# Kernel tuning notes

Measured on AMD Instinct MI355X. Metric: run time of the kernel, lower is better.

The kernel has to match this reference:

```python
import jax, jax.numpy as jnp
import numpy as np

B, T, VT, E, D = 128, 512, 2048, 1024, 1024  # batch, num_topics, topic_vocab, enc_hid, dec_hid


def setup_inputs() -> dict:
    key = jax.random.key(0)
    ks = jax.random.split(key, 8)
    # Split the Linear weight (in = dec_hid + topic_vocab + enc_hid, concat order: hidden, topic, enc)
    # into per-input blocks; math is identical to Linear(cat([h, t, e])).
    s = 1.0 / np.sqrt(D + VT + E)
    return {
        "hidden": jax.random.normal(ks[0], (B, D), jnp.float32),
        "topic_dict": jax.random.uniform(ks[1], (T, VT), jnp.float32),
        "enc_hidden": jax.random.normal(ks[2], (B, E), jnp.float32),
        "W_h": jax.random.uniform(ks[3], (D, D), jnp.float32, -s, s),
        "W_t": jax.random.uniform(ks[4], (VT, D), jnp.float32, -s, s),
        "W_e": jax.random.uniform(ks[5], (E, D), jnp.float32, -s, s),
        "b": jax.random.uniform(ks[6], (D,), jnp.float32, -s, s),
        "v": jax.random.uniform(ks[7], (D,), jnp.float32),
    }


def reference(hidden, topic_dict, enc_hidden, W_h, W_t, W_e, b, v):
    # Decompose Linear(cat(h, t, e)) = h@W_h + t@W_t + e@W_e + b; avoids the
    # repeated/concatenated [B, T, D+VT+E] buffer while computing the same math.
    h_proj = hidden @ W_h          # [B, D]
    t_proj = topic_dict @ W_t      # [T, D]
    e_proj = enc_hidden @ W_e      # [B, D]
    energy = jnp.tanh(h_proj[:, None, :] + e_proj[:, None, :] + t_proj[None, :, :] + b)  # [B, T, D]
    score = jnp.einsum("btd,d->bt", energy, v)  # [B, T]
    return jax.nn.softmax(score, axis=1)[:, None, :]  # [B, 1, T]
```

## Files before the change

### kernel.cpp

```cpp
#include <hip/hip_runtime.h>
#include <hip/hip_fp16.h>

#define B_ 128
#define T_ 512
#define VT_ 2048
#define E_ 1024
#define D_ 1024

typedef _Float16 h8 __attribute__((ext_vector_type(8)));
typedef float f4 __attribute__((ext_vector_type(4)));

#define C2LE 2.8853900817779268f
#define L2E  1.4426950408889634f

static __device__ __forceinline__ float rcpf(float x) { return __builtin_amdgcn_rcpf(x); }
static __device__ __forceinline__ float ex2(float x)  { return __builtin_amdgcn_exp2f(x); }

#define P_FLOATS   (8 * 640 * 1024)
#define R_FLOATS   (640 * 1024)
#define SP_FLOATS  (8 * 128 * 512)
#define PA_HALVES  (640 * 2048)
#define PB_WH      0
#define PB_WE      1048576
#define PB_WT      2097152

__device__ __forceinline__ void packA_do(const float* __restrict__ src, int ld, int KBs,
                                         _Float16* __restrict__ dst, int mb_off, int kb_off, int t)
{
    const int lane = t & 63;
    const int fb = t >> 6;
    const int kb = fb % KBs, mb = fb / KBs;
    const int r = lane & 15, g = lane >> 4;
    const float* s = src + (size_t)(mb * 16 + r) * ld + kb * 32 + g * 8;
    f4 v0 = *(const f4*)s, v1 = *(const f4*)(s + 4);
    h8 h;
    h[0] = (_Float16)v0[0]; h[1] = (_Float16)v0[1]; h[2] = (_Float16)v0[2]; h[3] = (_Float16)v0[3];
    h[4] = (_Float16)v1[0]; h[5] = (_Float16)v1[1]; h[6] = (_Float16)v1[2]; h[7] = (_Float16)v1[3];
    *(h8*)(dst + ((size_t)((mb_off + mb) * 64 + (kb_off + kb)) * 64 + lane) * 8) = h;
}

__device__ __forceinline__ void packB_do(const float* __restrict__ W, int KB,
                                         _Float16* __restrict__ dst, int t)
{
    const int lane = t & 63;
    const int fb = t >> 6;
    const int kb = fb % KB, nb = fb / KB;
    const int r = lane & 15, g = lane >> 4;
    const float* s = W + (size_t)(kb * 32 + g * 8) * 1024 + nb * 16 + r;
    h8 h;
    #pragma unroll
    for (int j = 0; j < 8; ++j) h[j] = (_Float16)s[(size_t)j * 1024];
    *(h8*)(dst + ((size_t)(nb * KB + kb) * 64 + lane) * 8) = h;
}

__global__ __launch_bounds__(256) void pack_kernel(
    const float* __restrict__ hidden, const float* __restrict__ topic,
    const float* __restrict__ enc,
    const float* __restrict__ W_h, const float* __restrict__ W_t, const float* __restrict__ W_e,
    _Float16* __restrict__ pA, _Float16* __restrict__ pB)
{
    const int bid = blockIdx.x, tid = threadIdx.x;
    if      (bid <   64) packA_do(hidden, 1024, 32, pA, 0,  0, bid * 256 + tid);
    else if (bid <  128) packA_do(enc,    1024, 32, pA, 0, 32, (bid -  64) * 256 + tid);
    else if (bid <  640) packA_do(topic,  2048, 64, pA, 8,  0, (bid - 128) * 256 + tid);
    else if (bid < 1152) packB_do(W_h, 32, pB + PB_WH, (bid -  640) * 256 + tid);
    else if (bid < 1664) packB_do(W_e, 32, pB + PB_WE, (bid - 1152) * 256 + tid);
    else                 packB_do(W_t, 64, pB + PB_WT, (bid - 1664) * 256 + tid);
}

__global__ __launch_bounds__(256, 3) void gemm_kernel(const _Float16* __restrict__ pA,
                                                      const _Float16* __restrict__ pB,
                                                      float* __restrict__ P)
{
    const int lin = blockIdx.x;
    const int sw  = (lin & 7) * 80 + (lin >> 3);
    const int s   = sw / 80;
    const int rem = sw % 80;
    const int mt  = rem % 10;
    const int nt  = rem / 10;

    const int tid = threadIdx.x, wave = tid >> 6, lane = tid & 63;
    const int wm = (wave >> 1) * 32;
    const int wn = (wave & 1) * 64;
    const int r = lane & 15, g = lane >> 4;

    const int mb0 = mt * 4 + (wm >> 4);
    const int nb0 = (nt * 128 + wn) >> 4;
    const int kb0 = s * 8;

    const _Float16* Bp; int KB_B, kbB0;
    if (mt < 2) {
        if (kb0 < 32) { Bp = pB + PB_WH; kbB0 = kb0; }
        else          { Bp = pB + PB_WE; kbB0 = kb0 - 32; }
        KB_B = 32;
    } else { Bp = pB + PB_WT; kbB0 = kb0; KB_B = 64; }

    const _Float16* Ap = pA + ((size_t)(mb0 * 64 + kb0) * 64 + lane) * 8;
    const _Float16* Bq = Bp + ((size_t)(nb0 * KB_B + kbB0) * 64 + lane) * 8;
    const size_t aStrM = (size_t)64 * 512;
    const size_t bStrN = (size_t)KB_B * 512;

    f4 acc[2][4] = {};
    #pragma unroll
    for (int ks = 0; ks < 8; ++ks) {
        h8 a0 = *(const h8*)(Ap + (size_t)ks * 512);
        h8 a1 = *(const h8*)(Ap + aStrM + (size_t)ks * 512);
        h8 b0 = *(const h8*)(Bq + (size_t)ks * 512);
        h8 b1 = *(const h8*)(Bq + bStrN + (size_t)ks * 512);
        h8 b2 = *(const h8*)(Bq + 2 * bStrN + (size_t)ks * 512);
        h8 b3 = *(const h8*)(Bq + 3 * bStrN + (size_t)ks * 512);
        acc[0][0] = __builtin_amdgcn_mfma_f32_16x16x32_f16(a0, b0, acc[0][0], 0, 0, 0);
        acc[0][1] = __builtin_amdgcn_mfma_f32_16x16x32_f16(a0, b1, acc[0][1], 0, 0, 0);
        acc[0][2] = __builtin_amdgcn_mfma_f32_16x16x32_f16(a0, b2, acc[0][2], 0, 0, 0);
        acc[0][3] = __builtin_amdgcn_mfma_f32_16x16x32_f16(a0, b3, acc[0][3], 0, 0, 0);
        acc[1][0] = __builtin_amdgcn_mfma_f32_16x16x32_f16(a1, b0, acc[1][0], 0, 0, 0);
        acc[1][1] = __builtin_amdgcn_mfma_f32_16x16x32_f16(a1, b1, acc[1][1], 0, 0, 0);
        acc[1][2] = __builtin_amdgcn_mfma_f32_16x16x32_f16(a1, b2, acc[1][2], 0, 0, 0);
        acc[1][3] = __builtin_amdgcn_mfma_f32_16x16x32_f16(a1, b3, acc[1][3], 0, 0, 0);
    }

    float* Pp = P + ((size_t)s * 640 + mt * 64 + wm + g * 4) * 1024 + nt * 128 + wn + r;
    #pragma unroll
    for (int i = 0; i < 2; ++i)
        #pragma unroll
        for (int j = 0; j < 4; ++j)
            #pragma unroll
            for (int q = 0; q < 4; ++q)
                Pp[(size_t)(i * 16 + q) * 1024 + j * 16] = C2LE * acc[i][j][q];
}

__global__ __launch_bounds__(256) void reduce_kernel(const float* __restrict__ P,
                                                     const float* __restrict__ bias,
                                                     float* __restrict__ R)
{
    const int row = blockIdx.x, tid = threadIdx.x;
    const size_t off = (size_t)row * 1024 + tid * 4;
    const size_t PS = (size_t)640 * 1024;
    f4 acc = *(const f4*)&P[off];
    #pragma unroll
    for (int z = 1; z < 8; ++z) acc += *(const f4*)&P[off + (size_t)z * PS];
    if (row < 128) {
        f4 bb = *(const f4*)&bias[tid * 4];
        acc += bb * C2LE;
    }
    *(f4*)&R[off] = acc;
}

__global__ __launch_bounds__(256) void score_kernel(const float* __restrict__ R,
                                                    const float* __restrict__ v,
                                                    float* __restrict__ SP)
{
    __shared__ float Xs[16][128];
    __shared__ float Ys[64][128];
    __shared__ float vs[128];

    const int tid = threadIdx.x;
    const int b0 = blockIdx.x * 16;
    const int t0 = blockIdx.y * 64;
    const int d0 = blockIdx.z * 128;

    #pragma unroll
    for (int i = 0; i < 8; ++i) {
        int idx = tid + i * 256;
        int row = idx >> 5, c4 = idx & 31;
        f4 vv = *(const f4*)&R[(size_t)(128 + t0 + row) * 1024 + d0 + c4 * 4];
        *(f4*)&Ys[row][(c4 ^ (row & 15)) * 4] = vv;
    }
    #pragma unroll
    for (int i = 0; i < 2; ++i) {
        int idx = tid + i * 256;
        int row = idx >> 5, c4 = idx & 31;
        f4 vv = *(const f4*)&R[(size_t)(b0 + row) * 1024 + d0 + c4 * 4];
        *(f4*)&Xs[row][(c4 ^ (row & 15)) * 4] = vv;
    }
    if (tid < 32) *(f4*)&vs[tid * 4] = *(const f4*)&v[d0 + tid * 4];
    __syncthreads();

    const int tq = tid & 31, bq = tid >> 5;
    const int sx0 = bq & 15, sx1 = (bq + 8) & 15, sy = tq & 15;
    float a00 = 0.f, a01 = 0.f, a10 = 0.f, a11 = 0.f;

    for (int dd = 0; dd < 32; ++dd) {
        f4 xa = *(const f4*)&Xs[bq]     [(dd ^ sx0) * 4];
        f4 xb = *(const f4*)&Xs[bq + 8] [(dd ^ sx1) * 4];
        f4 ya = *(const f4*)&Ys[tq]     [(dd ^ sy) * 4];
        f4 yb = *(const f4*)&Ys[tq + 32][(dd ^ sy) * 4];
        f4 vv = *(const f4*)&vs[dd * 4];
        #pragma unroll
        for (int j = 0; j < 4; ++j) {
            float e;
            e = ex2(xa[j] + ya[j]); a00 += vv[j] * rcpf(e + 1.0f);
            e = ex2(xa[j] + yb[j]); a01 += vv[j] * rcpf(e + 1.0f);
            e = ex2(xb[j] + ya[j]); a10 += vv[j] * rcpf(e + 1.0f);
            e = ex2(xb[j] + yb[j]); a11 += vv[j] * rcpf(e + 1.0f);
        }
    }

    float* sp = SP + (size_t)blockIdx.z * (B_ * T_);
    sp[(size_t)(b0 + bq)     * T_ + t0 + tq]      = a00;
    sp[(size_t)(b0 + bq)     * T_ + t0 + tq + 32] = a01;
    sp[(size_t)(b0 + bq + 8) * T_ + t0 + tq]      = a10;
    sp[(size_t)(b0 + bq + 8) * T_ + t0 + tq + 32] = a11;
}

__global__ __launch_bounds__(256) void softmax_kernel(
    const float* __restrict__ SP, float* __restrict__ out)
{
    const int b = blockIdx.x, tid = threadIdx.x;
    float s0 = 0.f, s1 = 0.f;
    #pragma unroll
    for (int z = 0; z < 8; ++z) {
        s0 += SP[(size_t)z * B_ * T_ + (size_t)b * T_ + tid];
        s1 += SP[(size_t)z * B_ * T_ + (size_t)b * T_ + tid + 256];
    }
    s0 *= -2.0f; s1 *= -2.0f;

    float m = fmaxf(s0, s1);
    #pragma unroll
    for (int off = 32; off >= 1; off >>= 1) m = fmaxf(m, __shfl_xor(m, off));
    __shared__ float red[4];
    __shared__ float red2[4];
    const int wv = tid >> 6;
    if ((tid & 63) == 0) red[wv] = m;
    __syncthreads();
    m = fmaxf(fmaxf(red[0], red[1]), fmaxf(red[2], red[3]));

    float e0 = ex2((s0 - m) * L2E);
    float e1 = ex2((s1 - m) * L2E);
    float sum = e0 + e1;
    #pragma unroll
    for (int off = 32; off >= 1; off >>= 1) sum += __shfl_xor(sum, off);
    if ((tid & 63) == 0) red2[wv] = sum;
    __syncthreads();
    sum = red2[0] + red2[1] + red2[2] + red2[3];

    const float rs = rcpf(sum);
    out[(size_t)b * T_ + tid]       = e0 * rs;
    out[(size_t)b * T_ + tid + 256] = e1 * rs;
}

extern "C" void kernel_launch(void* const* d_in, const int* in_sizes, int n_in,
                              void* d_out, int out_size, void* d_ws, size_t ws_size,
                              hipStream_t stream)
{
    const float* hidden = (const float*)d_in[0];
    const float* topic  = (const float*)d_in[1];
    const float* enc    = (const float*)d_in[2];
    const float* W_h    = (const float*)d_in[3];
    const float* W_t    = (const float*)d_in[4];
    const float* W_e    = (const float*)d_in[5];
    const float* bvec   = (const float*)d_in[6];
    const float* vvec   = (const float*)d_in[7];
    float* out = (float*)d_out;

    float* P      = (float*)d_ws;
    float* R      = P + P_FLOATS;
    float* SPb    = R + R_FLOATS;
    _Float16* pA  = (_Float16*)(SPb + SP_FLOATS);
    _Float16* pB  = pA + PA_HALVES;

    pack_kernel<<<2688, 256, 0, stream>>>(hidden, topic, enc, W_h, W_t, W_e, pA, pB);
    gemm_kernel<<<640, 256, 0, stream>>>(pA, pB, P);
    reduce_kernel<<<640, 256, 0, stream>>>(P, bvec, R);
    score_kernel<<<dim3(8, 8, 8), 256, 0, stream>>>(R, vvec, SPb);
    softmax_kernel<<<128, 256, 0, stream>>>(SPb, out);
}
```

Before: 115.0 us.

## Replace split-K partial buffer with atomic accumulation and LDS-staged packing

The GEMM's eight split-K slices now atomically add into a zeroed result buffer instead of writing separate partials, which removes the reduce kernel and its read of the partial buffer. The bias add moves into the score kernel. The pack kernel stages 64x64 panels through shared memory so both the A and weight conversions read global memory coalesced, rather than doing strided column reads for the weights. Costs are a memset launch, contention on the float atomics, and a summation order that is no longer deterministic.

After: 124.5 us. +8.3%, slower.

```diff
diff --git a/kernel.cpp b/kernel.cpp
--- a/kernel.cpp
+++ b/kernel.cpp
@@ -16,7 +16,6 @@
 static __device__ __forceinline__ float rcpf(float x) { return __builtin_amdgcn_rcpf(x); }
 static __device__ __forceinline__ float ex2(float x)  { return __builtin_amdgcn_exp2f(x); }
 
-#define P_FLOATS   (8 * 640 * 1024)
 #define R_FLOATS   (640 * 1024)
 #define SP_FLOATS  (8 * 128 * 512)
 #define PA_HALVES  (640 * 2048)
@@ -24,33 +23,55 @@
 #define PB_WE      1048576
 #define PB_WT      2097152
 
-__device__ __forceinline__ void packA_do(const float* __restrict__ src, int ld, int KBs,
-                                         _Float16* __restrict__ dst, int mb_off, int kb_off, int t)
-{
-    const int lane = t & 63;
-    const int fb = t >> 6;
-    const int kb = fb % KBs, mb = fb / KBs;
-    const int r = lane & 15, g = lane >> 4;
-    const float* s = src + (size_t)(mb * 16 + r) * ld + kb * 32 + g * 8;
-    f4 v0 = *(const f4*)s, v1 = *(const f4*)(s + 4);
-    h8 h;
-    h[0] = (_Float16)v0[0]; h[1] = (_Float16)v0[1]; h[2] = (_Float16)v0[2]; h[3] = (_Float16)v0[3];
-    h[4] = (_Float16)v1[0]; h[5] = (_Float16)v1[1]; h[6] = (_Float16)v1[2]; h[7] = (_Float16)v1[3];
-    *(h8*)(dst + ((size_t)((mb_off + mb) * 64 + (kb_off + kb)) * 64 + lane) * 8) = h;
-}
-
-__device__ __forceinline__ void packB_do(const float* __restrict__ W, int KB,
-                                         _Float16* __restrict__ dst, int t)
-{
-    const int lane = t & 63;
-    const int fb = t >> 6;
-    const int kb = fb % KB, nb = fb / KB;
-    const int r = lane & 15, g = lane >> 4;
-    const float* s = W + (size_t)(kb * 32 + g * 8) * 1024 + nb * 16 + r;
-    h8 h;
-    #pragma unroll
-    for (int j = 0; j < 8; ++j) h[j] = (_Float16)s[(size_t)j * 1024];
-    *(h8*)(dst + ((size_t)(nb * KB + kb) * 64 + lane) * 8) = h;
+__device__ __forceinline__ void pack_panelA(const float* __restrict__ src, int ld,
+                                            _Float16* __restrict__ dst, int mb_off, int kb_off,
+                                            int pm, int pk, int tid, float lds[64][72])
+{
+    #pragma unroll
+    for (int p = 0; p < 4; ++p) {
+        int row = (tid >> 4) + p * 16, col = (tid & 15) * 4;
+        *(f4*)&lds[row][col] = *(const f4*)&src[(size_t)(pm * 64 + row) * ld + pk * 64 + col];
+    }
+    __syncthreads();
+    #pragma unroll
+    for (int w = 0; w < 2; ++w) {
+        int fl = w * 256 + tid;
+        int f = fl >> 6, lane = fl & 63;
+        int i = f >> 1, k2 = f & 1;
+        int r = lane & 15, g = lane >> 4;
+        const float* p = &lds[i * 16 + r][k2 * 32 + g * 8];
+        h8 h;
+        #pragma unroll
+        for (int j = 0; j < 8; ++j) h[j] = (_Float16)p[j];
+        int MB = mb_off + pm * 4 + i;
+        int KB = kb_off + pk * 2 + k2;
+        *(h8*)(dst + ((size_t)(MB * 64 + KB) * 64 + lane) * 8) = h;
+    }
+}
+
+__device__ __forceinline__ void pack_panelB(const float* __restrict__ W,
+                                            _Float16* __restrict__ dst, int KBdim,
+                                            int pk, int pn, int tid, float lds[64][72])
+{
+    #pragma unroll
+    for (int p = 0; p < 4; ++p) {
+        int row = (tid >> 4) + p * 16, col = (tid & 15) * 4;
+        *(f4*)&lds[row][col] = *(const f4*)&W[(size_t)(pk * 64 + row) * 1024 + pn * 64 + col];
+    }
+    __syncthreads();
+    #pragma unroll
+    for (int w = 0; w < 2; ++w) {
+        int fl = w * 256 + tid;
+        int f = fl >> 6, lane = fl & 63;
+        int j = f >> 1, i2 = f & 1;
+        int r = lane & 15, g = lane >> 4;
+        h8 h;
+        #pragma unroll
+        for (int jj = 0; jj < 8; ++jj) h[jj] = (_Float16)lds[i2 * 32 + g * 8 + jj][j * 16 + r];
+        int NB = pn * 4 + j;
+        int KB = pk * 2 + i2;
+        *(h8*)(dst + ((size_t)(NB * KBdim + KB) * 64 + lane) * 8) = h;
+    }
 }
 
 __global__ __launch_bounds__(256) void pack_kernel(
@@ -59,18 +80,26 @@
     const float* __restrict__ W_h, const float* __restrict__ W_t, const float* __restrict__ W_e,
     _Float16* __restrict__ pA, _Float16* __restrict__ pB)
 {
+    __shared__ float lds[64][72];
     const int bid = blockIdx.x, tid = threadIdx.x;
-    if      (bid <   64) packA_do(hidden, 1024, 32, pA, 0,  0, bid * 256 + tid);
-    else if (bid <  128) packA_do(enc,    1024, 32, pA, 0, 32, (bid -  64) * 256 + tid);
-    else if (bid <  640) packA_do(topic,  2048, 64, pA, 8,  0, (bid - 128) * 256 + tid);
-    else if (bid < 1152) packB_do(W_h, 32, pB + PB_WH, (bid -  640) * 256 + tid);
-    else if (bid < 1664) packB_do(W_e, 32, pB + PB_WE, (bid - 1152) * 256 + tid);
-    else                 packB_do(W_t, 64, pB + PB_WT, (bid - 1664) * 256 + tid);
+    if (bid < 32) {
+        int b = bid;        pack_panelA(hidden, 1024, pA, 0,  0, b >> 4, b & 15, tid, lds);
+    } else if (bid < 64) {
+        int b = bid - 32;   pack_panelA(enc,    1024, pA, 0, 32, b >> 4, b & 15, tid, lds);
+    } else if (bid < 320) {
+        int b = bid - 64;   pack_panelA(topic,  2048, pA, 8,  0, b >> 5, b & 31, tid, lds);
+    } else if (bid < 576) {
+        int b = bid - 320;  pack_panelB(W_h, pB + PB_WH, 32, b >> 4, b & 15, tid, lds);
+    } else if (bid < 832) {
+        int b = bid - 576;  pack_panelB(W_e, pB + PB_WE, 32, b >> 4, b & 15, tid, lds);
+    } else {
+        int b = bid - 832;  pack_panelB(W_t, pB + PB_WT, 64, b >> 4, b & 15, tid, lds);
+    }
 }
 
 __global__ __launch_bounds__(256, 3) void gemm_kernel(const _Float16* __restrict__ pA,
                                                       const _Float16* __restrict__ pB,
-                                                      float* __restrict__ P)
+                                                      float* __restrict__ R)
 {
     const int lin = blockIdx.x;
     const int sw  = (lin & 7) * 80 + (lin >> 3);
@@ -119,34 +148,18 @@
         acc[1][3] = __builtin_amdgcn_mfma_f32_16x16x32_f16(a1, b3, acc[1][3], 0, 0, 0);
     }
 
-    float* Pp = P + ((size_t)s * 640 + mt * 64 + wm + g * 4) * 1024 + nt * 128 + wn + r;
+    float* Rp = R + ((size_t)(mt * 64 + wm + g * 4)) * 1024 + nt * 128 + wn + r;
     #pragma unroll
     for (int i = 0; i < 2; ++i)
         #pragma unroll
         for (int j = 0; j < 4; ++j)
             #pragma unroll
             for (int q = 0; q < 4; ++q)
-                Pp[(size_t)(i * 16 + q) * 1024 + j * 16] = C2LE * acc[i][j][q];
-}
-
-__global__ __launch_bounds__(256) void reduce_kernel(const float* __restrict__ P,
-                                                     const float* __restrict__ bias,
-                                                     float* __restrict__ R)
-{
-    const int row = blockIdx.x, tid = threadIdx.x;
-    const size_t off = (size_t)row * 1024 + tid * 4;
-    const size_t PS = (size_t)640 * 1024;
-    f4 acc = *(const f4*)&P[off];
-    #pragma unroll
-    for (int z = 1; z < 8; ++z) acc += *(const f4*)&P[off + (size_t)z * PS];
-    if (row < 128) {
-        f4 bb = *(const f4*)&bias[tid * 4];
-        acc += bb * C2LE;
-    }
-    *(f4*)&R[off] = acc;
+                atomicAdd(&Rp[(size_t)(i * 16 + q) * 1024 + j * 16], C2LE * acc[i][j][q]);
 }
 
 __global__ __launch_bounds__(256) void score_kernel(const float* __restrict__ R,
+                                                    const float* __restrict__ bias,
                                                     const float* __restrict__ v,
                                                     float* __restrict__ SP)
 {
@@ -171,6 +184,8 @@
         int idx = tid + i * 256;
         int row = idx >> 5, c4 = idx & 31;
         f4 vv = *(const f4*)&R[(size_t)(b0 + row) * 1024 + d0 + c4 * 4];
+        f4 bb = *(const f4*)&bias[d0 + c4 * 4];
+        vv += bb * C2LE;
         *(f4*)&Xs[row][(c4 ^ (row & 15)) * 4] = vv;
     }
     if (tid < 32) *(f4*)&vs[tid * 4] = *(const f4*)&v[d0 + tid * 4];
@@ -253,15 +268,14 @@
     const float* vvec   = (const float*)d_in[7];
     float* out = (float*)d_out;
 
-    float* P      = (float*)d_ws;
-    float* R      = P + P_FLOATS;
+    float* R      = (float*)d_ws;
     float* SPb    = R + R_FLOATS;
     _Float16* pA  = (_Float16*)(SPb + SP_FLOATS);
     _Float16* pB  = pA + PA_HALVES;
 
-    pack_kernel<<<2688, 256, 0, stream>>>(hidden, topic, enc, W_h, W_t, W_e, pA, pB);
-    gemm_kernel<<<640, 256, 0, stream>>>(pA, pB, P);
-    reduce_kernel<<<640, 256, 0, stream>>>(P, bvec, R);
-    score_kernel<<<dim3(8, 8, 8), 256, 0, stream>>>(R, vvec, SPb);
+    (void)hipMemsetAsync(R, 0, R_FLOATS * sizeof(float), stream);
+    pack_kernel<<<1344, 256, 0, stream>>>(hidden, topic, enc, W_h, W_t, W_e, pA, pB);
+    gemm_kernel<<<640, 256, 0, stream>>>(pA, pB, R);
+    score_kernel<<<dim3(8, 8, 8), 256, 0, stream>>>(R, bvec, vvec, SPb);
     softmax_kernel<<<128, 256, 0, stream>>>(SPb, out);
 }
```
